# Kernel tuning notes

Hardware: AMD Instinct MI355X
Metric: run time of the kernel (lower is better)

Reference implementation:

```python
import jax, jax.numpy as jnp
import numpy as np

N = 20000   # genes
E = 200000  # global edges
P = 300     # pathways
EP = 2000   # edges per pathway (global node indices)
D = 3       # in_dim == number of omics (forced by nn.Linear(3,1))


def setup_inputs():
    key = jax.random.key(0)
    ks = jax.random.split(key, 20)
    f = lambda i, shape: jax.random.normal(ks[i], shape, dtype=jnp.float32) * 0.1
    return {
        "x": f(0, (N, D)),
        "edge_index": jax.random.randint(ks[1], (2, E), 0, N),
        "path_edges": jax.random.randint(ks[2], (P, 2, EP), 0, N),
        "W_pool": f(3, (D, D)), "b_pool": f(4, (D,)),
        "W_self": f(5, (D, D)), "W_neigh": f(6, (D, D)), "b_conv": f(7, (D,)),
        "sub_Wl": f(8, (P, D, D)), "sub_bl": f(9, (P, D)), "sub_Wr": f(10, (P, D, D)),
        "pool_Wrel": f(11, (P, D, 1)), "pool_Wroot": f(12, (P, D, 1)), "pool_b": f(13, (P, 1)),
        "gate_W": f(14, (P, D, 1)), "gate_b": f(15, (P, 1)),
        "lin_W": f(16, (D, 1)), "lin_b": f(17, (1,)),
        "mlp_W": f(18, (P, 1)), "mlp_b": f(19, (1,)),
    }


def reference(x, edge_index, path_edges, W_pool, b_pool, W_self, W_neigh, b_conv,
              sub_Wl, sub_bl, sub_Wr, pool_Wrel, pool_Wroot, pool_b,
              gate_W, gate_b, lin_W, lin_b, mlp_W, mlp_b):
    n = x.shape[0]
    # add_self_loops on the global edge_index
    loops = jnp.arange(n)
    src = jnp.concatenate([edge_index[0], loops])
    dst = jnp.concatenate([edge_index[1], loops])

    # global SAGEConv with 'pool' aggregator: max_j relu(W_pool h_j), then self + neigh
    hp = jax.nn.relu(x @ W_pool + b_pool)                       # [N,D]
    agg = jax.ops.segment_max(hp[src], dst, num_segments=n)     # [N,D] (self-loops -> no empty segments)
    h = jnp.tanh(x @ W_self + agg @ W_neigh + b_conv)           # [N,D]

    k = int(np.ceil(0.8 * n))  # SAGPooling ratio=0.8 over all N nodes (full x is passed per pathway)

    def per_path(pe, Wl, bl, Wr, Wrel, Wroot, pb, gW, gb):
        s, d = pe[0], pe[1]
        # SAGEConv (mean aggr) on pathway subgraph edges over full node set
        msum = jax.ops.segment_sum(h[s], d, num_segments=n)
        cnt = jax.ops.segment_sum(jnp.ones(s.shape, h.dtype), d, num_segments=n)
        mean = msum / jnp.maximum(cnt, 1.0)[:, None]
        xc = jax.nn.relu(mean @ Wl + bl + h @ Wr)               # [N,D]
        # SAGPooling score via GraphConv (add aggr): W_rel * sum_j x_j + W_root * x + b
        asum = jax.ops.segment_sum(xc[s], d, num_segments=n)
        score = (asum @ Wrel + xc @ Wroot + pb)[:, 0]           # [N]
        topv, perm = jax.lax.top_k(score, k)
        xk = xc[perm] * jnp.tanh(topv)[:, None]                 # [k,D]
        # GlobalAttention readout: softmax gate over kept nodes
        gate = jax.nn.softmax((xk @ gW + gb)[:, 0])             # [k]
        return jax.nn.relu(gate @ xk)                            # [D]

    readout = jax.vmap(per_path)(path_edges, sub_Wl, sub_bl, sub_Wr,
                                 pool_Wrel, pool_Wroot, pool_b, gate_W, gate_b)  # [P,D]
    r = jax.nn.relu(readout @ lin_W + lin_b).T                  # [1,P]
    # mlp: Dropout (identity in eval) -> ReLU -> Linear(P,1) -> Sigmoid
    return jax.nn.sigmoid(jax.nn.relu(r) @ mlp_W + mlp_b)       # [1,1]
```

## Files before the change

kernel.cpp:

```cpp
#include <hip/hip_runtime.h>
#include <math.h>

#define MAXM 2048
#define BMW  640
#define BS   1024
#define NB   2048

__device__ __forceinline__ unsigned fkey(float f){
  unsigned u = __float_as_uint(f);
  return (u & 0x80000000u) ? ~u : (u | 0x80000000u);
}
__device__ __forceinline__ int lbin(float sc, float lo, float scl){
  int b = (int)((sc - lo) * scl);
  return b < 0 ? 0 : (b > NB-1 ? NB-1 : b);
}
__device__ __forceinline__ void hp_eval(const float* __restrict__ x, int i,
                                        const float* __restrict__ Wp,
                                        const float* __restrict__ bp, float* o){
  float x0 = x[i*3+0], x1 = x[i*3+1], x2 = x[i*3+2];
  #pragma unroll
  for (int j = 0; j < 3; ++j)
    o[j] = fmaxf(x0*Wp[0*3+j] + x1*Wp[1*3+j] + x2*Wp[2*3+j] + bp[j], 0.f);
}

__global__ void k_edge(const float* __restrict__ x, const int* __restrict__ ei,
                       const float* __restrict__ Wp, const float* __restrict__ bp,
                       float* __restrict__ agg, float* __restrict__ acc,
                       unsigned* __restrict__ counter, int E){
  if (blockIdx.x == 0 && threadIdx.x == 0){ acc[0] = 0.f; counter[0] = 0u; }
  int e = blockIdx.x*blockDim.x + threadIdx.x;
  if (e >= E) return;
  int s = ei[e], d = ei[E+e];
  float o[3]; hp_eval(x, s, Wp, bp, o);
  #pragma unroll
  for (int j = 0; j < 3; ++j)
    atomicMax((int*)&agg[d*3+j], __float_as_int(o[j]));
}

__global__ void k_h2(const float* __restrict__ x, float* __restrict__ hb,
                     const float* __restrict__ Wp, const float* __restrict__ bp,
                     const float* __restrict__ Ws, const float* __restrict__ Wn,
                     const float* __restrict__ bc, int N){
  int i = blockIdx.x*blockDim.x + threadIdx.x;
  if (i >= N) return;
  float hp[3]; hp_eval(x, i, Wp, bp, hp);
  float x0 = x[i*3+0], x1 = x[i*3+1], x2 = x[i*3+2];
  float a0 = fmaxf(hb[i*3+0], hp[0]);
  float a1 = fmaxf(hb[i*3+1], hp[1]);
  float a2 = fmaxf(hb[i*3+2], hp[2]);
  float o[3];
  #pragma unroll
  for (int j = 0; j < 3; ++j){
    float v = x0*Ws[0*3+j] + x1*Ws[1*3+j] + x2*Ws[2*3+j]
            + a0*Wn[0*3+j] + a1*Wn[1*3+j] + a2*Wn[2*3+j] + bc[j];
    o[j] = tanhf(v);
  }
  hb[i*3+0] = o[0]; hb[i*3+1] = o[1]; hb[i*3+2] = o[2];
}

__device__ __forceinline__ void pick_bucket(const unsigned* hist, int l,
    unsigned pref, unsigned mask, int shift,
    unsigned* sel_prefix, unsigned* sel_mask, int* sel_r){
  unsigned h0 = hist[4*l+0], h1 = hist[4*l+1], h2 = hist[4*l+2], h3 = hist[4*l+3];
  unsigned s = h0+h1+h2+h3;
  unsigned S = s;
  #pragma unroll
  for (int off = 1; off < 64; off <<= 1){
    unsigned t = __shfl_down(S, off);
    if (l + off < 64) S += t;
  }
  unsigned Snext = S - s;
  unsigned r = (unsigned)*sel_r;
  unsigned suf3 = h3 + Snext;
  unsigned suf2 = h2 + suf3;
  unsigned suf1 = h1 + suf2;
  unsigned suf0 = h0 + suf1;
  int b = -1; unsigned sufnext = 0;
  if      (suf3 >= r && Snext < r){ b = 4*l+3; sufnext = Snext; }
  else if (suf2 >= r && suf3  < r){ b = 4*l+2; sufnext = suf3; }
  else if (suf1 >= r && suf2  < r){ b = 4*l+1; sufnext = suf2; }
  else if (suf0 >= r && suf1  < r){ b = 4*l+0; sufnext = suf1; }
  if (b >= 0){
    *sel_prefix = pref | ((unsigned)b << shift);
    *sel_mask   = mask | (255u << shift);
    *sel_r      = (int)(r - sufnext);
  }
}

__global__ void __launch_bounds__(BS)
k_mega(const float* __restrict__ h, const int* __restrict__ pe,
       const float* __restrict__ sWl, const float* __restrict__ sbl, const float* __restrict__ sWr,
       const float* __restrict__ pWrel, const float* __restrict__ pWroot, const float* __restrict__ pB,
       const float* __restrict__ gW, const float* __restrict__ gB,
       const float* __restrict__ linW, const float* __restrict__ linb,
       const float* __restrict__ mlpW, const float* __restrict__ mlpb,
       float* __restrict__ spG, float* __restrict__ acc, unsigned* __restrict__ counter,
       unsigned* __restrict__ out, int N, int EP, int K, int P){
  __shared__ unsigned bm[BMW];
  __shared__ int      wpfx[BMW];
  __shared__ float    msum[MAXM*3];
  __shared__ unsigned scrA[NB];
  __shared__ unsigned scrB[NB];
  __shared__ float    wredf[(BS/64)*4];
  __shared__ float    s_mn, s_mx;
  __shared__ float    rlo[3], rsc[3];
  __shared__ int      rb[3];
  __shared__ int      s_r, s_C, s_cc, s_done;
  __shared__ unsigned s_uT;
  __shared__ unsigned sel_prefix, sel_mask;
  __shared__ int      sel_r;

  const int p = blockIdx.x;
  const int tid = threadIdx.x;

  float Wl[9], Wr[9], bl[3], wrel[3], wroot[3], gw[3];
  #pragma unroll
  for (int j = 0; j < 9; ++j){ Wl[j] = sWl[p*9+j]; Wr[j] = sWr[p*9+j]; }
  #pragma unroll
  for (int j = 0; j < 3; ++j){
    bl[j] = sbl[p*3+j]; wrel[j] = pWrel[p*3+j];
    wroot[j] = pWroot[p*3+j]; gw[j] = gW[p*3+j];
  }
  float pbv = pB[p], gbv = gB[p];
  float* sp = spG + (size_t)p*N;

  int*   cnt  = (int*)scrA;
  float* adot = (float*)scrB;

  for (int s = tid; s < MAXM; s += BS){
    cnt[s] = 0; adot[s] = 0.f;
    msum[s*3+0]=0.f; msum[s*3+1]=0.f; msum[s*3+2]=0.f;
  }
  for (int s = tid; s < BMW; s += BS) bm[s] = 0u;
  if (tid == 0){ s_done = 0; s_uT = 0u; }
  __syncthreads();

  const int* ps = pe + (size_t)p*2*EP;
  const int* pd = ps + EP;

  for (int e = tid; e < EP; e += BS) atomicOr(&bm[pd[e]>>5], 1u << (pd[e]&31));
  __syncthreads();
  if (tid < 64){
    int l = tid, base = l*10;
    int c[10], s = 0;
    #pragma unroll
    for (int q = 0; q < 10; ++q){ c[q] = __popc(bm[base+q]); s += c[q]; }
    int pre = s;
    #pragma unroll
    for (int off = 1; off < 64; off <<= 1){
      int t = __shfl_up(pre, off);
      if (l >= off) pre += t;
    }
    pre -= s;
    #pragma unroll
    for (int q = 0; q < 10; ++q){ wpfx[base+q] = pre; pre += c[q]; }
  }
  __syncthreads();
  for (int e = tid; e < EP; e += BS){
    int s = ps[e], d = pd[e];
    int r = wpfx[d>>5] + __popc(bm[d>>5] & ((1u << (d&31)) - 1u));
    atomicAdd(&cnt[r], 1);
    atomicAdd(&msum[r*3+0], h[s*3+0]);
    atomicAdd(&msum[r*3+1], h[s*3+1]);
    atomicAdd(&msum[r*3+2], h[s*3+2]);
  }
  __syncthreads();
  for (int r = tid; r < MAXM; r += BS){
    int c = cnt[r];
    if (c > 0){
      float inv = 1.f / (float)c;
      msum[r*3+0] *= inv; msum[r*3+1] *= inv; msum[r*3+2] *= inv;
    }
  }
  __syncthreads();
  for (int e = tid; e < EP; e += BS){
    int s = ps[e], d = pd[e];
    float m0=0.f,m1=0.f,m2=0.f;
    unsigned w = bm[s>>5];
    if ((w >> (s&31)) & 1u){
      int rs = wpfx[s>>5] + __popc(w & ((1u << (s&31)) - 1u));
      m0 = msum[rs*3+0]; m1 = msum[rs*3+1]; m2 = msum[rs*3+2];
    }
    float h0 = h[s*3+0], h1 = h[s*3+1], h2 = h[s*3+2];
    float x0 = fmaxf(m0*Wl[0]+m1*Wl[3]+m2*Wl[6] + bl[0] + h0*Wr[0]+h1*Wr[3]+h2*Wr[6], 0.f);
    float x1 = fmaxf(m0*Wl[1]+m1*Wl[4]+m2*Wl[7] + bl[1] + h0*Wr[1]+h1*Wr[4]+h2*Wr[7], 0.f);
    float x2 = fmaxf(m0*Wl[2]+m1*Wl[5]+m2*Wl[8] + bl[2] + h0*Wr[2]+h1*Wr[5]+h2*Wr[8], 0.f);
    int rd = wpfx[d>>5] + __popc(bm[d>>5] & ((1u << (d&31)) - 1u));
    atomicAdd(&adot[rd], x0*wrel[0] + x1*wrel[1] + x2*wrel[2]);
  }
  __syncthreads();

  float mn = 3.0e38f, mx = -3.0e38f;
  for (int i = tid; i < N; i += BS){
    float m0=0.f,m1=0.f,m2=0.f,ad=0.f;
    unsigned w = bm[i>>5];
    if ((w >> (i&31)) & 1u){
      int r = wpfx[i>>5] + __popc(w & ((1u << (i&31)) - 1u));
      m0 = msum[r*3+0]; m1 = msum[r*3+1]; m2 = msum[r*3+2];
      ad = adot[r];
    }
    float h0 = h[i*3+0], h1 = h[i*3+1], h2 = h[i*3+2];
    float x0 = fmaxf(m0*Wl[0]+m1*Wl[3]+m2*Wl[6] + bl[0] + h0*Wr[0]+h1*Wr[3]+h2*Wr[6], 0.f);
    float x1 = fmaxf(m0*Wl[1]+m1*Wl[4]+m2*Wl[7] + bl[1] + h0*Wr[1]+h1*Wr[4]+h2*Wr[7], 0.f);
    float x2 = fmaxf(m0*Wl[2]+m1*Wl[5]+m2*Wl[8] + bl[2] + h0*Wr[2]+h1*Wr[5]+h2*Wr[8], 0.f);
    float sc = ad + x0*wroot[0]+x1*wroot[1]+x2*wroot[2] + pbv;
    sp[i] = sc;
    mn = fminf(mn, sc); mx = fmaxf(mx, sc);
  }
  #pragma unroll
  for (int off = 32; off > 0; off >>= 1){
    mn = fminf(mn, __shfl_down(mn, off));
    mx = fmaxf(mx, __shfl_down(mx, off));
  }
  if ((tid & 63) == 0){ int w = tid>>6; wredf[w*2+0] = mn; wredf[w*2+1] = mx; }
  __syncthreads();
  if (tid == 0){
    float a = 3.0e38f, b = -3.0e38f;
    for (int w = 0; w < BS/64; ++w){ a = fminf(a, wredf[w*2+0]); b = fmaxf(b, wredf[w*2+1]); }
    s_mn = a; s_mx = b; s_r = K;
    if (!(b > a)){ s_uT = fkey(a); s_done = 1; }
  }
  __syncthreads();

  unsigned* hist = scrA;
  unsigned* cand = scrB;

  for (int t = 0; t < 3; ++t){
    __syncthreads();
    if (s_done) break;
    float lo, hi;
    if (t == 0){ lo = s_mn; hi = s_mx; }
    else { lo = rlo[t-1] + rb[t-1]/rsc[t-1]; hi = rlo[t-1] + (rb[t-1]+1)/rsc[t-1]; }
    float scl = 2047.0f / (hi - lo);
    if (!(hi > lo) || !(scl < 1e37f)){
      if (tid == 0){ s_uT = fkey(lo); s_done = 1; }
      __syncthreads();
      continue;
    }
    for (int b = tid; b < NB; b += BS) hist[b] = 0u;
    __syncthreads();
    if (t == 0){
      if ((N & 3) == 0){
        int G = N >> 2;
        for (int g = tid; g < G; g += BS){
          float4 v = ((const float4*)sp)[g];
          atomicAdd(&hist[lbin(v.x, lo, scl)], 1u);
          atomicAdd(&hist[lbin(v.y, lo, scl)], 1u);
          atomicAdd(&hist[lbin(v.z, lo, scl)], 1u);
          atomicAdd(&hist[lbin(v.w, lo, scl)], 1u);
        }
      } else {
        for (int i = tid; i < N; i += BS) atomicAdd(&hist[lbin(sp[i], lo, scl)], 1u);
      }
    } else {
      for (int i = tid; i < N; i += BS){
        float sc = sp[i];
        bool act = true;
        for (int q = 0; q < t; ++q) act = act && (lbin(sc, rlo[q], rsc[q]) == rb[q]);
        if (act) atomicAdd(&hist[lbin(sc, lo, scl)], 1u);
      }
    }
    __syncthreads();
    if (tid < 64){
      int l = tid;
      unsigned s = 0;
      for (int q = 0; q < 32; ++q) s += hist[l*32+q];
      unsigned S = s;
      #pragma unroll
      for (int off = 1; off < 64; off <<= 1){
        unsigned u2 = __shfl_down(S, off);
        if (l + off < 64) S += u2;
      }
      unsigned suf = S - s;
      unsigned r = (unsigned)s_r;
      int b = -1; unsigned sufnext = 0, cb = 0;
      for (int q = 31; q >= 0; --q){
        unsigned c = hist[l*32+q];
        unsigned nsuf = suf + c;
        if (nsuf >= r && suf < r){ b = l*32+q; sufnext = suf; cb = c; }
        suf = nsuf;
      }
      if (b >= 0){
        rb[t] = b; rlo[t] = lo; rsc[t] = scl;
        s_r = (int)(r - sufnext);
        s_C = (int)cb;
      }
    }
    __syncthreads();
    int C = s_C;
    if (C <= NB){
      if (tid == 0) s_cc = 0;
      __syncthreads();
      for (int i = tid; i < N; i += BS){
        float sc = sp[i];
        bool act = true;
        for (int q = 0; q <= t; ++q) act = act && (lbin(sc, rlo[q], rsc[q]) == rb[q]);
        if (act){ int ix = atomicAdd(&s_cc, 1); if (ix < NB) cand[ix] = fkey(sc); }
      }
      __syncthreads();
      if (tid == 0){ sel_prefix = 0u; sel_mask = 0u; sel_r = s_r; }
      __syncthreads();
      for (int pass = 0; pass < 4; ++pass){
        int shift = 24 - 8*pass;
        if (tid < 256) hist[tid] = 0u;
        __syncthreads();
        unsigned mask = sel_mask, pref = sel_prefix;
        for (int j = tid; j < C; j += BS){
          unsigned u = cand[j];
          if ((u & mask) == pref) atomicAdd(&hist[(u>>shift)&255u], 1u);
        }
        __syncthreads();
        if (tid < 64)
          pick_bucket(hist, tid, pref, mask, shift, &sel_prefix, &sel_mask, &sel_r);
        __syncthreads();
      }
      if (tid == 0){ s_uT = sel_prefix; s_done = 1; }
      __syncthreads();
    } else if (t == 2){
      if (tid == 0){ s_uT = fkey(lo + rb[t]/scl); s_done = 1; }
      __syncthreads();
    }
  }
  __syncthreads();
  const unsigned uT = s_uT;

  float l = 0.f, a0 = 0.f, a1 = 0.f, a2 = 0.f;
  for (int i = tid; i < N; i += BS){
    float sc = sp[i];
    if (fkey(sc) >= uT){
      float m0=0.f,m1=0.f,m2=0.f;
      unsigned w = bm[i>>5];
      if ((w >> (i&31)) & 1u){
        int r = wpfx[i>>5] + __popc(w & ((1u << (i&31)) - 1u));
        m0 = msum[r*3+0]; m1 = msum[r*3+1]; m2 = msum[r*3+2];
      }
      float h0 = h[i*3+0], h1 = h[i*3+1], h2 = h[i*3+2];
      float x0 = fmaxf(m0*Wl[0]+m1*Wl[3]+m2*Wl[6] + bl[0] + h0*Wr[0]+h1*Wr[3]+h2*Wr[6], 0.f);
      float x1 = fmaxf(m0*Wl[1]+m1*Wl[4]+m2*Wl[7] + bl[1] + h0*Wr[1]+h1*Wr[4]+h2*Wr[7], 0.f);
      float x2 = fmaxf(m0*Wl[2]+m1*Wl[5]+m2*Wl[8] + bl[2] + h0*Wr[2]+h1*Wr[5]+h2*Wr[8], 0.f);
      float tt = tanhf(sc);
      x0 *= tt; x1 *= tt; x2 *= tt;
      float g = x0*gw[0] + x1*gw[1] + x2*gw[2] + gbv;
      g = fminf(fmaxf(g, -60.f), 60.f);
      float e = expf(g);
      l += e; a0 += e*x0; a1 += e*x1; a2 += e*x2;
    }
  }
  #pragma unroll
  for (int off = 32; off > 0; off >>= 1){
    l  += __shfl_down(l,  off);
    a0 += __shfl_down(a0, off);
    a1 += __shfl_down(a1, off);
    a2 += __shfl_down(a2, off);
  }
  if ((tid & 63) == 0){
    int w = tid >> 6;
    wredf[w*4+0]=l; wredf[w*4+1]=a0; wredf[w*4+2]=a1; wredf[w*4+3]=a2;
  }
  __syncthreads();
  if (tid == 0){
    float L=0.f, A0=0.f, A1=0.f, A2=0.f;
    for (int w = 0; w < BS/64; ++w){
      L += wredf[w*4+0]; A0 += wredf[w*4+1]; A1 += wredf[w*4+2]; A2 += wredf[w*4+3];
    }
    float inv = 1.f / L;
    float r0 = fmaxf(A0*inv, 0.f);
    float r1 = fmaxf(A1*inv, 0.f);
    float r2 = fmaxf(A2*inv, 0.f);
    float rr = fmaxf(r0*linW[0] + r1*linW[1] + r2*linW[2] + linb[0], 0.f);
    atomicAdd(acc, rr * mlpW[p]);
    __threadfence();
    unsigned old = atomicAdd(counter, 1u);
    if (old == (unsigned)(P-1)){
      __threadfence();
      float z = atomicAdd(acc, 0.f) + mlpb[0];
      float a = 1.f / (1.f + expf(-z));
      unsigned A = __float_as_uint(a);
      unsigned B = (A + 0x7FFFu + ((A >> 16) & 1u)) >> 16;
      out[0] = (A & 0xFFFF0000u) | (B & 0xFFFFu);
    }
  }
}

extern "C" void kernel_launch(void* const* d_in, const int* in_sizes, int n_in,
                              void* d_out, int out_size, void* d_ws, size_t ws_size,
                              hipStream_t stream){
  const float* x      = (const float*)d_in[0];
  const int*   ei     = (const int*)  d_in[1];
  const int*   pe     = (const int*)  d_in[2];
  const float* W_pool = (const float*)d_in[3];
  const float* b_pool = (const float*)d_in[4];
  const float* W_self = (const float*)d_in[5];
  const float* W_neigh= (const float*)d_in[6];
  const float* b_conv = (const float*)d_in[7];
  const float* sWl    = (const float*)d_in[8];
  const float* sbl    = (const float*)d_in[9];
  const float* sWr    = (const float*)d_in[10];
  const float* pWrel  = (const float*)d_in[11];
  const float* pWroot = (const float*)d_in[12];
  const float* pB     = (const float*)d_in[13];
  const float* gW     = (const float*)d_in[14];
  const float* gB     = (const float*)d_in[15];
  const float* linW   = (const float*)d_in[16];
  const float* linb   = (const float*)d_in[17];
  const float* mlpW   = (const float*)d_in[18];
  const float* mlpb   = (const float*)d_in[19];

  const int N  = in_sizes[0] / 3;
  const int E  = in_sizes[1] / 2;
  const int P  = in_sizes[13];
  const int EP = in_sizes[2] / (2 * P);
  const int K  = (4*N + 4) / 5;

  float*    ws      = (float*)d_ws;
  float*    acc     = ws;
  unsigned* counter = (unsigned*)(ws + 1);
  float*    agg     = ws + 16;
  float*    h       = agg;
  float*    spG     = ws + 16 + (size_t)3*N;

  k_edge<<<(E+255)/256, 256, 0, stream>>>(x, ei, W_pool, b_pool, agg, acc, counter, E);
  k_h2  <<<(N+255)/256, 256, 0, stream>>>(x, agg, W_pool, b_pool,
                                          W_self, W_neigh, b_conv, N);
  k_mega<<<P, BS, 0, stream>>>(h, pe, sWl, sbl, sWr, pWrel, pWroot, pB, gW, gB,
                               linW, linb, mlpW, mlpb,
                               spG, acc, counter, (unsigned*)d_out, N, EP, K, P);
}
```

Before: 252.8 us.

## Pad h to float4 and keep per-thread scores in registers across selection passes

```diff
diff --git a/kernel.cpp b/kernel.cpp
--- a/kernel.cpp
+++ b/kernel.cpp
@@ -4,6 +4,7 @@
 #define MAXM 2048
 #define BMW  640
 #define BS   1024
+#define NPT  20
 #define NB   2048
 
 __device__ __forceinline__ unsigned fkey(float f){
@@ -37,7 +38,8 @@
     atomicMax((int*)&agg[d*3+j], __float_as_int(o[j]));
 }
 
-__global__ void k_h2(const float* __restrict__ x, float* __restrict__ hb,
+__global__ void k_h2(const float* __restrict__ x, const float* __restrict__ agg,
+                     float4* __restrict__ h4,
                      const float* __restrict__ Wp, const float* __restrict__ bp,
                      const float* __restrict__ Ws, const float* __restrict__ Wn,
                      const float* __restrict__ bc, int N){
@@ -45,9 +47,9 @@
   if (i >= N) return;
   float hp[3]; hp_eval(x, i, Wp, bp, hp);
   float x0 = x[i*3+0], x1 = x[i*3+1], x2 = x[i*3+2];
-  float a0 = fmaxf(hb[i*3+0], hp[0]);
-  float a1 = fmaxf(hb[i*3+1], hp[1]);
-  float a2 = fmaxf(hb[i*3+2], hp[2]);
+  float a0 = fmaxf(agg[i*3+0], hp[0]);
+  float a1 = fmaxf(agg[i*3+1], hp[1]);
+  float a2 = fmaxf(agg[i*3+2], hp[2]);
   float o[3];
   #pragma unroll
   for (int j = 0; j < 3; ++j){
@@ -55,7 +57,7 @@
             + a0*Wn[0*3+j] + a1*Wn[1*3+j] + a2*Wn[2*3+j] + bc[j];
     o[j] = tanhf(v);
   }
-  hb[i*3+0] = o[0]; hb[i*3+1] = o[1]; hb[i*3+2] = o[2];
+  h4[i] = make_float4(o[0], o[1], o[2], 0.f);
 }
 
 __device__ __forceinline__ void pick_bucket(const unsigned* hist, int l,
@@ -88,7 +90,7 @@
 }
 
 __global__ void __launch_bounds__(BS)
-k_mega(const float* __restrict__ h, const int* __restrict__ pe,
+k_mega(const float4* __restrict__ h4, const int* __restrict__ pe,
        const float* __restrict__ sWl, const float* __restrict__ sbl, const float* __restrict__ sWr,
        const float* __restrict__ pWrel, const float* __restrict__ pWroot, const float* __restrict__ pB,
        const float* __restrict__ gW, const float* __restrict__ gB,
@@ -159,10 +161,11 @@
   for (int e = tid; e < EP; e += BS){
     int s = ps[e], d = pd[e];
     int r = wpfx[d>>5] + __popc(bm[d>>5] & ((1u << (d&31)) - 1u));
+    float4 hv = h4[s];
     atomicAdd(&cnt[r], 1);
-    atomicAdd(&msum[r*3+0], h[s*3+0]);
-    atomicAdd(&msum[r*3+1], h[s*3+1]);
-    atomicAdd(&msum[r*3+2], h[s*3+2]);
+    atomicAdd(&msum[r*3+0], hv.x);
+    atomicAdd(&msum[r*3+1], hv.y);
+    atomicAdd(&msum[r*3+2], hv.z);
   }
   __syncthreads();
   for (int r = tid; r < MAXM; r += BS){
@@ -181,17 +184,39 @@
       int rs = wpfx[s>>5] + __popc(w & ((1u << (s&31)) - 1u));
       m0 = msum[rs*3+0]; m1 = msum[rs*3+1]; m2 = msum[rs*3+2];
     }
-    float h0 = h[s*3+0], h1 = h[s*3+1], h2 = h[s*3+2];
-    float x0 = fmaxf(m0*Wl[0]+m1*Wl[3]+m2*Wl[6] + bl[0] + h0*Wr[0]+h1*Wr[3]+h2*Wr[6], 0.f);
-    float x1 = fmaxf(m0*Wl[1]+m1*Wl[4]+m2*Wl[7] + bl[1] + h0*Wr[1]+h1*Wr[4]+h2*Wr[7], 0.f);
-    float x2 = fmaxf(m0*Wl[2]+m1*Wl[5]+m2*Wl[8] + bl[2] + h0*Wr[2]+h1*Wr[5]+h2*Wr[8], 0.f);
+    float4 hv = h4[s];
+    float x0 = fmaxf(m0*Wl[0]+m1*Wl[3]+m2*Wl[6] + bl[0] + hv.x*Wr[0]+hv.y*Wr[3]+hv.z*Wr[6], 0.f);
+    float x1 = fmaxf(m0*Wl[1]+m1*Wl[4]+m2*Wl[7] + bl[1] + hv.x*Wr[1]+hv.y*Wr[4]+hv.z*Wr[7], 0.f);
+    float x2 = fmaxf(m0*Wl[2]+m1*Wl[5]+m2*Wl[8] + bl[2] + hv.x*Wr[2]+hv.y*Wr[5]+hv.z*Wr[8], 0.f);
     int rd = wpfx[d>>5] + __popc(bm[d>>5] & ((1u << (d&31)) - 1u));
     atomicAdd(&adot[rd], x0*wrel[0] + x1*wrel[1] + x2*wrel[2]);
   }
   __syncthreads();
 
+  float scq[NPT];
   float mn = 3.0e38f, mx = -3.0e38f;
-  for (int i = tid; i < N; i += BS){
+  #pragma unroll
+  for (int j = 0; j < NPT; ++j){
+    int i = tid + j*BS;
+    float sc = 0.f;
+    if (i < N){
+      float m0=0.f,m1=0.f,m2=0.f,ad=0.f;
+      unsigned w = bm[i>>5];
+      if ((w >> (i&31)) & 1u){
+        int r = wpfx[i>>5] + __popc(w & ((1u << (i&31)) - 1u));
+        m0 = msum[r*3+0]; m1 = msum[r*3+1]; m2 = msum[r*3+2];
+        ad = adot[r];
+      }
+      float4 hv = h4[i];
+      float x0 = fmaxf(m0*Wl[0]+m1*Wl[3]+m2*Wl[6] + bl[0] + hv.x*Wr[0]+hv.y*Wr[3]+hv.z*Wr[6], 0.f);
+      float x1 = fmaxf(m0*Wl[1]+m1*Wl[4]+m2*Wl[7] + bl[1] + hv.x*Wr[1]+hv.y*Wr[4]+hv.z*Wr[7], 0.f);
+      float x2 = fmaxf(m0*Wl[2]+m1*Wl[5]+m2*Wl[8] + bl[2] + hv.x*Wr[2]+hv.y*Wr[5]+hv.z*Wr[8], 0.f);
+      sc = ad + x0*wroot[0]+x1*wroot[1]+x2*wroot[2] + pbv;
+      mn = fminf(mn, sc); mx = fmaxf(mx, sc);
+    }
+    scq[j] = sc;
+  }
+  for (int i = BS*NPT + tid; i < N; i += BS){
     float m0=0.f,m1=0.f,m2=0.f,ad=0.f;
     unsigned w = bm[i>>5];
     if ((w >> (i&31)) & 1u){
@@ -199,10 +224,10 @@
       m0 = msum[r*3+0]; m1 = msum[r*3+1]; m2 = msum[r*3+2];
       ad = adot[r];
     }
-    float h0 = h[i*3+0], h1 = h[i*3+1], h2 = h[i*3+2];
-    float x0 = fmaxf(m0*Wl[0]+m1*Wl[3]+m2*Wl[6] + bl[0] + h0*Wr[0]+h1*Wr[3]+h2*Wr[6], 0.f);
-    float x1 = fmaxf(m0*Wl[1]+m1*Wl[4]+m2*Wl[7] + bl[1] + h0*Wr[1]+h1*Wr[4]+h2*Wr[7], 0.f);
-    float x2 = fmaxf(m0*Wl[2]+m1*Wl[5]+m2*Wl[8] + bl[2] + h0*Wr[2]+h1*Wr[5]+h2*Wr[8], 0.f);
+    float4 hv = h4[i];
+    float x0 = fmaxf(m0*Wl[0]+m1*Wl[3]+m2*Wl[6] + bl[0] + hv.x*Wr[0]+hv.y*Wr[3]+hv.z*Wr[6], 0.f);
+    float x1 = fmaxf(m0*Wl[1]+m1*Wl[4]+m2*Wl[7] + bl[1] + hv.x*Wr[1]+hv.y*Wr[4]+hv.z*Wr[7], 0.f);
+    float x2 = fmaxf(m0*Wl[2]+m1*Wl[5]+m2*Wl[8] + bl[2] + hv.x*Wr[2]+hv.y*Wr[5]+hv.z*Wr[8], 0.f);
     float sc = ad + x0*wroot[0]+x1*wroot[1]+x2*wroot[2] + pbv;
     sp[i] = sc;
     mn = fminf(mn, sc); mx = fmaxf(mx, sc);
@@ -239,26 +264,21 @@
     }
     for (int b = tid; b < NB; b += BS) hist[b] = 0u;
     __syncthreads();
-    if (t == 0){
-      if ((N & 3) == 0){
-        int G = N >> 2;
-        for (int g = tid; g < G; g += BS){
-          float4 v = ((const float4*)sp)[g];
-          atomicAdd(&hist[lbin(v.x, lo, scl)], 1u);
-          atomicAdd(&hist[lbin(v.y, lo, scl)], 1u);
-          atomicAdd(&hist[lbin(v.z, lo, scl)], 1u);
-          atomicAdd(&hist[lbin(v.w, lo, scl)], 1u);
-        }
-      } else {
-        for (int i = tid; i < N; i += BS) atomicAdd(&hist[lbin(sp[i], lo, scl)], 1u);
-      }
-    } else {
-      for (int i = tid; i < N; i += BS){
-        float sc = sp[i];
+    #pragma unroll
+    for (int j = 0; j < NPT; ++j){
+      int i = tid + j*BS;
+      if (i < N){
+        float sc = scq[j];
         bool act = true;
         for (int q = 0; q < t; ++q) act = act && (lbin(sc, rlo[q], rsc[q]) == rb[q]);
         if (act) atomicAdd(&hist[lbin(sc, lo, scl)], 1u);
       }
+    }
+    for (int i = BS*NPT + tid; i < N; i += BS){
+      float sc = sp[i];
+      bool act = true;
+      for (int q = 0; q < t; ++q) act = act && (lbin(sc, rlo[q], rsc[q]) == rb[q]);
+      if (act) atomicAdd(&hist[lbin(sc, lo, scl)], 1u);
     }
     __syncthreads();
     if (tid < 64){
@@ -291,7 +311,17 @@
     if (C <= NB){
       if (tid == 0) s_cc = 0;
       __syncthreads();
-      for (int i = tid; i < N; i += BS){
+      #pragma unroll
+      for (int j = 0; j < NPT; ++j){
+        int i = tid + j*BS;
+        if (i < N){
+          float sc = scq[j];
+          bool act = true;
+          for (int q = 0; q <= t; ++q) act = act && (lbin(sc, rlo[q], rsc[q]) == rb[q]);
+          if (act){ int ix = atomicAdd(&s_cc, 1); if (ix < NB) cand[ix] = fkey(sc); }
+        }
+      }
+      for (int i = BS*NPT + tid; i < N; i += BS){
         float sc = sp[i];
         bool act = true;
         for (int q = 0; q <= t; ++q) act = act && (lbin(sc, rlo[q], rsc[q]) == rb[q]);
@@ -325,7 +355,30 @@
   const unsigned uT = s_uT;
 
   float l = 0.f, a0 = 0.f, a1 = 0.f, a2 = 0.f;
-  for (int i = tid; i < N; i += BS){
+  #pragma unroll
+  for (int j = 0; j < NPT; ++j){
+    int i = tid + j*BS;
+    if (i < N && fkey(scq[j]) >= uT){
+      float sc = scq[j];
+      float m0=0.f,m1=0.f,m2=0.f;
+      unsigned w = bm[i>>5];
+      if ((w >> (i&31)) & 1u){
+        int r = wpfx[i>>5] + __popc(w & ((1u << (i&31)) - 1u));
+        m0 = msum[r*3+0]; m1 = msum[r*3+1]; m2 = msum[r*3+2];
+      }
+      float4 hv = h4[i];
+      float x0 = fmaxf(m0*Wl[0]+m1*Wl[3]+m2*Wl[6] + bl[0] + hv.x*Wr[0]+hv.y*Wr[3]+hv.z*Wr[6], 0.f);
+      float x1 = fmaxf(m0*Wl[1]+m1*Wl[4]+m2*Wl[7] + bl[1] + hv.x*Wr[1]+hv.y*Wr[4]+hv.z*Wr[7], 0.f);
+      float x2 = fmaxf(m0*Wl[2]+m1*Wl[5]+m2*Wl[8] + bl[2] + hv.x*Wr[2]+hv.y*Wr[5]+hv.z*Wr[8], 0.f);
+      float tt = tanhf(sc);
+      x0 *= tt; x1 *= tt; x2 *= tt;
+      float g = x0*gw[0] + x1*gw[1] + x2*gw[2] + gbv;
+      g = fminf(fmaxf(g, -60.f), 60.f);
+      float e = expf(g);
+      l += e; a0 += e*x0; a1 += e*x1; a2 += e*x2;
+    }
+  }
+  for (int i = BS*NPT + tid; i < N; i += BS){
     float sc = sp[i];
     if (fkey(sc) >= uT){
       float m0=0.f,m1=0.f,m2=0.f;
@@ -334,10 +387,10 @@
         int r = wpfx[i>>5] + __popc(w & ((1u << (i&31)) - 1u));
         m0 = msum[r*3+0]; m1 = msum[r*3+1]; m2 = msum[r*3+2];
       }
-      float h0 = h[i*3+0], h1 = h[i*3+1], h2 = h[i*3+2];
-      float x0 = fmaxf(m0*Wl[0]+m1*Wl[3]+m2*Wl[6] + bl[0] + h0*Wr[0]+h1*Wr[3]+h2*Wr[6], 0.f);
-      float x1 = fmaxf(m0*Wl[1]+m1*Wl[4]+m2*Wl[7] + bl[1] + h0*Wr[1]+h1*Wr[4]+h2*Wr[7], 0.f);
-      float x2 = fmaxf(m0*Wl[2]+m1*Wl[5]+m2*Wl[8] + bl[2] + h0*Wr[2]+h1*Wr[5]+h2*Wr[8], 0.f);
+      float4 hv = h4[i];
+      float x0 = fmaxf(m0*Wl[0]+m1*Wl[3]+m2*Wl[6] + bl[0] + hv.x*Wr[0]+hv.y*Wr[3]+hv.z*Wr[6], 0.f);
+      float x1 = fmaxf(m0*Wl[1]+m1*Wl[4]+m2*Wl[7] + bl[1] + hv.x*Wr[1]+hv.y*Wr[4]+hv.z*Wr[7], 0.f);
+      float x2 = fmaxf(m0*Wl[2]+m1*Wl[5]+m2*Wl[8] + bl[2] + hv.x*Wr[2]+hv.y*Wr[5]+hv.z*Wr[8], 0.f);
       float tt = tanhf(sc);
       x0 *= tt; x1 *= tt; x2 *= tt;
       float g = x0*gw[0] + x1*gw[1] + x2*gw[2] + gbv;
@@ -416,13 +469,14 @@
   float*    acc     = ws;
   unsigned* counter = (unsigned*)(ws + 1);
   float*    agg     = ws + 16;
-  float*    h       = agg;
-  float*    spG     = ws + 16 + (size_t)3*N;
+  size_t    o_h4    = (16 + (size_t)3*N + 3) & ~(size_t)3;
+  float4*   h4      = (float4*)(ws + o_h4);
+  float*    spG     = ws + o_h4 + (size_t)4*N;
 
   k_edge<<<(E+255)/256, 256, 0, stream>>>(x, ei, W_pool, b_pool, agg, acc, counter, E);
-  k_h2  <<<(N+255)/256, 256, 0, stream>>>(x, agg, W_pool, b_pool,
+  k_h2  <<<(N+255)/256, 256, 0, stream>>>(x, agg, h4, W_pool, b_pool,
                                           W_self, W_neigh, b_conv, N);
-  k_mega<<<P, BS, 0, stream>>>(h, pe, sWl, sbl, sWr, pWrel, pWroot, pB, gW, gB,
+  k_mega<<<P, BS, 0, stream>>>(h4, pe, sWl, sbl, sWr, pWrel, pWroot, pB, gW, gB,
                                linW, linb, mlpW, mlpb,
                                spG, acc, counter, (unsigned*)d_out, N, EP, K, P);
 }
```

After: 255.5 us. Within noise of the previous version (+1.1%).
